# Performance work log

Hardware: AMD Instinct MI355X
Metric: run time of the kernel (lower is better)

Reference implementation:

```python
import jax, jax.numpy as jnp
import numpy as np

def mish(x):
    return x * jnp.tanh(jax.nn.softplus(x))

def setup_inputs() -> dict:
    ANT, RF, DS, G, B = 64, 8, 8, 16, 4096
    BB_DIM = 2 * RF * DS      # 128
    RF_DIM = 2 * ANT * RF     # 1024
    key = jax.random.key(0)
    ks = jax.random.split(key, 10)
    def lin(kw, kb, i, o):
        lim = 1.0 / np.sqrt(i)
        W = jax.random.uniform(kw, (o, i), jnp.float32, -lim, lim)
        b = jax.random.uniform(kb, (o,), jnp.float32, -lim, lim)
        return W, b
    W_rfbb, b_rfbb = lin(ks[0], ks[1], RF_DIM, BB_DIM)
    W_rfrf, b_rfrf = lin(ks[2], ks[3], RF_DIM, RF_DIM)
    W_bbrf, b_bbrf = lin(ks[4], ks[5], BB_DIM, RF_DIM)
    W_bbbb, b_bbbb = lin(ks[6], ks[7], BB_DIM, BB_DIM)
    BB_feature = jax.random.normal(ks[8], (B, G, BB_DIM), jnp.float32)
    RF_feature = jax.random.normal(ks[9], (B, RF_DIM), jnp.float32)
    return {
        "BB_feature": BB_feature, "RF_feature": RF_feature,
        "W_rfbb": W_rfbb, "b_rfbb": b_rfbb,
        "W_rfrf": W_rfrf, "b_rfrf": b_rfrf,
        "W_bbrf": W_bbrf, "b_bbrf": b_bbrf,
        "W_bbbb": W_bbbb, "b_bbbb": b_bbbb,
    }

def reference(BB_feature, RF_feature, W_rfbb, b_rfbb, W_rfrf, b_rfrf, W_bbrf, b_bbrf, W_bbbb, b_bbbb):
    # mean over subcarrier-group dim
    BB_mean = jnp.mean(BB_feature, axis=-2)                      # [B, BB_DIM]
    RF_to_RF = mish(RF_feature @ W_rfrf.T + b_rfrf)              # [B, RF_DIM]
    RF_to_BB = mish(RF_feature @ W_rfbb.T + b_rfbb)              # [B, BB_DIM]
    BB_to_RF = mish(BB_mean @ W_bbrf.T + b_bbrf)                 # [B, RF_DIM]
    BB_to_BB = mish(jnp.einsum('bgi,oi->bgo', BB_feature, W_bbbb) + b_bbbb)  # [B, G, BB_DIM]
    new_RF = RF_to_RF + BB_to_RF
    new_BB = BB_to_BB + RF_to_BB[:, None, :]
    return (new_BB, new_RF)
```

## Files before the change

kernel.cpp:

```cpp
#include <hip/hip_runtime.h>
#include <hip/hip_bf16.h>

typedef __attribute__((ext_vector_type(8))) short short8;
typedef __attribute__((ext_vector_type(4))) float floatx4;

#define BDIM 128
#define RDIM 1024
#define NB   4096
#define NG   16
#define LDP  40

__device__ __forceinline__ float mishf(float x) {
    float e = __expf(x);
    float t = e * (e + 2.0f);
    float r = x * (t / (t + 2.0f));
    return x > 20.0f ? x : r;
}

__device__ __forceinline__ short8 cvt8v(float4 f0, float4 f1) {
    union { __hip_bfloat162 h; unsigned u; } c0, c1, c2, c3;
    c0.h = __float22bfloat162_rn(make_float2(f0.x, f0.y));
    c1.h = __float22bfloat162_rn(make_float2(f0.z, f0.w));
    c2.h = __float22bfloat162_rn(make_float2(f1.x, f1.y));
    c3.h = __float22bfloat162_rn(make_float2(f1.z, f1.w));
    union { short8 s; unsigned u[4]; } r;
    r.u[0] = c0.u; r.u[1] = c1.u; r.u[2] = c2.u; r.u[3] = c3.u;
    return r.s;
}

#define MFMA(a, b, c) __builtin_amdgcn_mfma_f32_16x16x32_bf16(a, b, c, 0, 0, 0)

__global__ void __launch_bounds__(256) k_mean(const float* __restrict__ bb,
                                              float* __restrict__ mean) {
    int tid = blockIdx.x * blockDim.x + threadIdx.x;
    int b = tid >> 5;
    int d = (tid & 31) * 4;
    const float4* p = (const float4*)(bb + (size_t)b * (NG * BDIM) + d);
    float4 s = {0.f, 0.f, 0.f, 0.f};
    #pragma unroll
    for (int g = 0; g < NG; ++g) {
        float4 v = p[g * (BDIM / 4)];
        s.x += v.x; s.y += v.y; s.z += v.z; s.w += v.w;
    }
    s.x *= 0.0625f; s.y *= 0.0625f; s.z *= 0.0625f; s.w *= 0.0625f;
    *(float4*)(mean + (size_t)b * BDIM + d) = s;
}

__global__ void __launch_bounds__(256) k_rf2bb(
    const float* __restrict__ rf,
    const float* __restrict__ W,
    const float* __restrict__ bias,
    float* __restrict__ outw)
{
    __shared__ short As[16 * LDP];
    __shared__ short Bs[128 * LDP];
    int tid = threadIdx.x;
    int wave = tid >> 6, lane = tid & 63;
    int r = lane & 15, quad = lane >> 4;
    int m0 = blockIdx.x * 16;
    int srow = tid >> 2, sks = tid & 3;

    const float* aG  = rf + (size_t)(m0 + srow) * RDIM + sks * 8;
    const float* bG0 = W  + (size_t)srow * RDIM + sks * 8;
    const float* bG1 = W  + (size_t)(64 + srow) * RDIM + sks * 8;

    float4 qa0, qa1, qb00, qb01, qb10, qb11;
    if (tid < 64) { qa0 = *(const float4*)aG; qa1 = *(const float4*)(aG + 4); }
    qb00 = *(const float4*)bG0; qb01 = *(const float4*)(bG0 + 4);
    qb10 = *(const float4*)bG1; qb11 = *(const float4*)(bG1 + 4);

    floatx4 acc[2];
    acc[0] = floatx4{0.f,0.f,0.f,0.f}; acc[1] = acc[0];

    for (int it = 0; it < 32; ++it) {
        __syncthreads();
        if (tid < 64) *(short8*)&As[srow * LDP + sks * 8] = cvt8v(qa0, qa1);
        *(short8*)&Bs[srow * LDP + sks * 8]        = cvt8v(qb00, qb01);
        *(short8*)&Bs[(64 + srow) * LDP + sks * 8] = cvt8v(qb10, qb11);
        __syncthreads();
        if (it < 31) {
            int k = (it + 1) * 32;
            if (tid < 64) { qa0 = *(const float4*)(aG + k); qa1 = *(const float4*)(aG + k + 4); }
            qb00 = *(const float4*)(bG0 + k); qb01 = *(const float4*)(bG0 + k + 4);
            qb10 = *(const float4*)(bG1 + k); qb11 = *(const float4*)(bG1 + k + 4);
        }
        short8 a = *(short8*)&As[r * LDP + quad * 8];
        #pragma unroll
        for (int nj = 0; nj < 2; ++nj) {
            short8 b = *(short8*)&Bs[(wave * 32 + nj * 16 + r) * LDP + quad * 8];
            acc[nj] = MFMA(a, b, acc[nj]);
        }
    }
    #pragma unroll
    for (int nj = 0; nj < 2; ++nj) {
        int col = wave * 32 + nj * 16 + r;
        float bs = bias[col];
        #pragma unroll
        for (int g = 0; g < 4; ++g) {
            int row = m0 + quad * 4 + g;
            outw[(size_t)row * BDIM + col] = mishf(acc[nj][g] + bs);
        }
    }
}

__global__ void __launch_bounds__(512) k_newrf(
    const float* __restrict__ rf,
    const float* __restrict__ meanp,
    const float* __restrict__ Wrfrf,
    const float* __restrict__ brfrf,
    const float* __restrict__ Wbbrf,
    const float* __restrict__ bbbrf,
    float* __restrict__ out)
{
    __shared__ short As[128 * LDP];
    __shared__ short Bs[128 * LDP];
    int tid = threadIdx.x;
    int wave = tid >> 6, lane = tid & 63;
    int r = lane & 15, quad = lane >> 4;
    int w_m = (wave & 3) * 32, w_n = (wave >> 2) * 64;
    int mt = blockIdx.x >> 3, nt = blockIdx.x & 7;
    int m0 = mt * 128, n0 = nt * 128;
    int srow = tid >> 2, sks = tid & 3;
    int sidx = srow * LDP + sks * 8;

    const float* aG = rf    + (size_t)(m0 + srow) * RDIM + sks * 8;
    const float* bG = Wrfrf + (size_t)(n0 + srow) * RDIM + sks * 8;
    float4 pa0 = *(const float4*)aG, pa1 = *(const float4*)(aG + 4);
    float4 pb0 = *(const float4*)bG, pb1 = *(const float4*)(bG + 4);

    floatx4 acc1[2][4], acc2[2][4];
    #pragma unroll
    for (int i = 0; i < 2; ++i)
        #pragma unroll
        for (int j = 0; j < 4; ++j) { acc1[i][j] = floatx4{0.f,0.f,0.f,0.f}; acc2[i][j] = acc1[i][j]; }

    for (int it = 0; it < 32; ++it) {
        __syncthreads();
        *(short8*)&As[sidx] = cvt8v(pa0, pa1);
        *(short8*)&Bs[sidx] = cvt8v(pb0, pb1);
        __syncthreads();
        if (it < 31) {
            int k = (it + 1) * 32;
            pa0 = *(const float4*)(aG + k); pa1 = *(const float4*)(aG + k + 4);
            pb0 = *(const float4*)(bG + k); pb1 = *(const float4*)(bG + k + 4);
        }
        short8 a0 = *(short8*)&As[(w_m + r) * LDP + quad * 8];
        short8 a1 = *(short8*)&As[(w_m + 16 + r) * LDP + quad * 8];
        #pragma unroll
        for (int nj = 0; nj < 4; ++nj) {
            short8 b = *(short8*)&Bs[(w_n + nj * 16 + r) * LDP + quad * 8];
            acc1[0][nj] = MFMA(a0, b, acc1[0][nj]);
            acc1[1][nj] = MFMA(a1, b, acc1[1][nj]);
        }
    }

    const float* a2G = meanp + (size_t)(m0 + srow) * BDIM + sks * 8;
    const float* b2G = Wbbrf + (size_t)(n0 + srow) * BDIM + sks * 8;
    pa0 = *(const float4*)a2G; pa1 = *(const float4*)(a2G + 4);
    pb0 = *(const float4*)b2G; pb1 = *(const float4*)(b2G + 4);
    for (int it = 0; it < 4; ++it) {
        __syncthreads();
        *(short8*)&As[sidx] = cvt8v(pa0, pa1);
        *(short8*)&Bs[sidx] = cvt8v(pb0, pb1);
        __syncthreads();
        if (it < 3) {
            int k = (it + 1) * 32;
            pa0 = *(const float4*)(a2G + k); pa1 = *(const float4*)(a2G + k + 4);
            pb0 = *(const float4*)(b2G + k); pb1 = *(const float4*)(b2G + k + 4);
        }
        short8 a0 = *(short8*)&As[(w_m + r) * LDP + quad * 8];
        short8 a1 = *(short8*)&As[(w_m + 16 + r) * LDP + quad * 8];
        #pragma unroll
        for (int nj = 0; nj < 4; ++nj) {
            short8 b = *(short8*)&Bs[(w_n + nj * 16 + r) * LDP + quad * 8];
            acc2[0][nj] = MFMA(a0, b, acc2[0][nj]);
            acc2[1][nj] = MFMA(a1, b, acc2[1][nj]);
        }
    }

    #pragma unroll
    for (int mi = 0; mi < 2; ++mi) {
        #pragma unroll
        for (int nj = 0; nj < 4; ++nj) {
            int col = n0 + w_n + nj * 16 + r;
            float b1 = brfrf[col];
            float b2 = bbbrf[col];
            #pragma unroll
            for (int g = 0; g < 4; ++g) {
                int row = m0 + w_m + mi * 16 + quad * 4 + g;
                out[(size_t)row * RDIM + col] = mishf(acc1[mi][nj][g] + b1) + mishf(acc2[mi][nj][g] + b2);
            }
        }
    }
}

__global__ void __launch_bounds__(256) k_newbb(
    const float* __restrict__ bb,
    const float* __restrict__ W,
    const float* __restrict__ bias,
    const float* __restrict__ rf2bb,
    float* __restrict__ out)
{
    __shared__ short As[128 * LDP];
    __shared__ short Ws[128 * LDP];
    int tid = threadIdx.x;
    int wave = tid >> 6, lane = tid & 63;
    int r = lane & 15, quad = lane >> 4;
    size_t m0 = (size_t)blockIdx.x * 128;
    int srow = tid >> 2, sks = tid & 3;

    const float* aG0 = bb + (m0 + srow) * BDIM + sks * 8;
    const float* aG1 = bb + (m0 + 64 + srow) * BDIM + sks * 8;
    const float* wG0 = W + (size_t)srow * BDIM + sks * 8;
    const float* wG1 = W + (size_t)(64 + srow) * BDIM + sks * 8;

    float4 qa00 = *(const float4*)aG0, qa01 = *(const float4*)(aG0 + 4);
    float4 qa10 = *(const float4*)aG1, qa11 = *(const float4*)(aG1 + 4);
    float4 qw00 = *(const float4*)wG0, qw01 = *(const float4*)(wG0 + 4);
    float4 qw10 = *(const float4*)wG1, qw11 = *(const float4*)(wG1 + 4);

    floatx4 acc[2][8];
    #pragma unroll
    for (int i = 0; i < 2; ++i)
        #pragma unroll
        for (int j = 0; j < 8; ++j) acc[i][j] = floatx4{0.f,0.f,0.f,0.f};

    for (int kc = 0; kc < 4; ++kc) {
        __syncthreads();
        *(short8*)&As[srow * LDP + sks * 8]        = cvt8v(qa00, qa01);
        *(short8*)&As[(64 + srow) * LDP + sks * 8] = cvt8v(qa10, qa11);
        *(short8*)&Ws[srow * LDP + sks * 8]        = cvt8v(qw00, qw01);
        *(short8*)&Ws[(64 + srow) * LDP + sks * 8] = cvt8v(qw10, qw11);
        __syncthreads();
        if (kc < 3) {
            int k = (kc + 1) * 32;
            qa00 = *(const float4*)(aG0 + k); qa01 = *(const float4*)(aG0 + k + 4);
            qa10 = *(const float4*)(aG1 + k); qa11 = *(const float4*)(aG1 + k + 4);
            qw00 = *(const float4*)(wG0 + k); qw01 = *(const float4*)(wG0 + k + 4);
            qw10 = *(const float4*)(wG1 + k); qw11 = *(const float4*)(wG1 + k + 4);
        }
        short8 a0 = *(short8*)&As[(wave * 32 + r) * LDP + quad * 8];
        short8 a1 = *(short8*)&As[(wave * 32 + 16 + r) * LDP + quad * 8];
        #pragma unroll
        for (int nj = 0; nj < 8; ++nj) {
            short8 b = *(short8*)&Ws[(nj * 16 + r) * LDP + quad * 8];
            acc[0][nj] = MFMA(a0, b, acc[0][nj]);
            acc[1][nj] = MFMA(a1, b, acc[1][nj]);
        }
    }

    #pragma unroll
    for (int mi = 0; mi < 2; ++mi) {
        #pragma unroll
        for (int nj = 0; nj < 8; ++nj) {
            int col = nj * 16 + r;
            float bs = bias[col];
            #pragma unroll
            for (int g = 0; g < 4; ++g) {
                size_t row = m0 + wave * 32 + mi * 16 + quad * 4 + g;
                out[row * BDIM + col] = mishf(acc[mi][nj][g] + bs) + rf2bb[(row >> 4) * BDIM + col];
            }
        }
    }
}

extern "C" void kernel_launch(void* const* d_in, const int* in_sizes, int n_in,
                              void* d_out, int out_size, void* d_ws, size_t ws_size,
                              hipStream_t stream) {
    const float* BB    = (const float*)d_in[0];
    const float* RF    = (const float*)d_in[1];
    const float* Wrfbb = (const float*)d_in[2];
    const float* brfbb = (const float*)d_in[3];
    const float* Wrfrf = (const float*)d_in[4];
    const float* brfrf = (const float*)d_in[5];
    const float* Wbbrf = (const float*)d_in[6];
    const float* bbbrf = (const float*)d_in[7];
    const float* Wbbbb = (const float*)d_in[8];
    const float* bbbbb = (const float*)d_in[9];

    float* outBB = (float*)d_out;
    float* outRF = outBB + (size_t)NB * NG * BDIM;

    float* mean  = (float*)d_ws;
    float* rf2bb = (float*)((char*)d_ws + (size_t)NB * BDIM * 4);

    k_mean <<<512, 256, 0, stream>>>(BB, mean);
    k_rf2bb<<<256, 256, 0, stream>>>(RF, Wrfbb, brfbb, rf2bb);
    k_newrf<<<256, 512, 0, stream>>>(RF, mean, Wrfrf, brfrf, Wbbrf, bbbrf, outRF);
    k_newbb<<<512, 256, 0, stream>>>(BB, Wbbbb, bbbbb, rf2bb, outBB);
}
```

Before: 187.8 us.

## Fuse RF-to-BB GEMM into RF GEMM kernel and double-buffer LDS tiles

Removes the separate k_rf2bb kernel: the first 8 column tiles of k_newrf also compute the RF→BB projection, reusing the already-staged RF A-tiles against a 16-row slice of W_rfbb. The RF kernel's tiling changes to 128x64 tiles with 256 threads and 512 blocks, and LDS becomes double-buffered so each k-step needs one barrier instead of two. k_newbb now stages the full W_bbbb once into LDS and double-buffers only the activation tiles. The cost is load imbalance, since only half of the RF blocks and half of their waves do the extra MFMA work, plus more LDS per block.

Measured after the change: 162.6 us. 1.15x faster.

```diff
diff --git a/kernel.cpp b/kernel.cpp
--- a/kernel.cpp
+++ b/kernel.cpp
@@ -9,6 +9,7 @@
 #define NB   4096
 #define NG   16
 #define LDP  40
+#define WSTR 136
 
 __device__ __forceinline__ float mishf(float x) {
     float e = __expf(x);
@@ -46,149 +47,167 @@
     *(float4*)(mean + (size_t)b * BDIM + d) = s;
 }
 
-__global__ void __launch_bounds__(256) k_rf2bb(
-    const float* __restrict__ rf,
-    const float* __restrict__ W,
-    const float* __restrict__ bias,
-    float* __restrict__ outw)
-{
-    __shared__ short As[16 * LDP];
-    __shared__ short Bs[128 * LDP];
-    int tid = threadIdx.x;
-    int wave = tid >> 6, lane = tid & 63;
-    int r = lane & 15, quad = lane >> 4;
-    int m0 = blockIdx.x * 16;
-    int srow = tid >> 2, sks = tid & 3;
-
-    const float* aG  = rf + (size_t)(m0 + srow) * RDIM + sks * 8;
-    const float* bG0 = W  + (size_t)srow * RDIM + sks * 8;
-    const float* bG1 = W  + (size_t)(64 + srow) * RDIM + sks * 8;
-
-    float4 qa0, qa1, qb00, qb01, qb10, qb11;
-    if (tid < 64) { qa0 = *(const float4*)aG; qa1 = *(const float4*)(aG + 4); }
-    qb00 = *(const float4*)bG0; qb01 = *(const float4*)(bG0 + 4);
-    qb10 = *(const float4*)bG1; qb11 = *(const float4*)(bG1 + 4);
-
-    floatx4 acc[2];
-    acc[0] = floatx4{0.f,0.f,0.f,0.f}; acc[1] = acc[0];
-
-    for (int it = 0; it < 32; ++it) {
-        __syncthreads();
-        if (tid < 64) *(short8*)&As[srow * LDP + sks * 8] = cvt8v(qa0, qa1);
-        *(short8*)&Bs[srow * LDP + sks * 8]        = cvt8v(qb00, qb01);
-        *(short8*)&Bs[(64 + srow) * LDP + sks * 8] = cvt8v(qb10, qb11);
-        __syncthreads();
-        if (it < 31) {
-            int k = (it + 1) * 32;
-            if (tid < 64) { qa0 = *(const float4*)(aG + k); qa1 = *(const float4*)(aG + k + 4); }
-            qb00 = *(const float4*)(bG0 + k); qb01 = *(const float4*)(bG0 + k + 4);
-            qb10 = *(const float4*)(bG1 + k); qb11 = *(const float4*)(bG1 + k + 4);
-        }
-        short8 a = *(short8*)&As[r * LDP + quad * 8];
-        #pragma unroll
-        for (int nj = 0; nj < 2; ++nj) {
-            short8 b = *(short8*)&Bs[(wave * 32 + nj * 16 + r) * LDP + quad * 8];
-            acc[nj] = MFMA(a, b, acc[nj]);
-        }
-    }
-    #pragma unroll
-    for (int nj = 0; nj < 2; ++nj) {
-        int col = wave * 32 + nj * 16 + r;
-        float bs = bias[col];
-        #pragma unroll
-        for (int g = 0; g < 4; ++g) {
-            int row = m0 + quad * 4 + g;
-            outw[(size_t)row * BDIM + col] = mishf(acc[nj][g] + bs);
-        }
-    }
-}
-
-__global__ void __launch_bounds__(512) k_newrf(
+__global__ void __launch_bounds__(256) k_newrf(
     const float* __restrict__ rf,
     const float* __restrict__ meanp,
     const float* __restrict__ Wrfrf,
     const float* __restrict__ brfrf,
     const float* __restrict__ Wbbrf,
     const float* __restrict__ bbbrf,
-    float* __restrict__ out)
+    const float* __restrict__ Wrfbb,
+    const float* __restrict__ brfbb,
+    float* __restrict__ out,
+    float* __restrict__ rf2bb)
 {
-    __shared__ short As[128 * LDP];
-    __shared__ short Bs[128 * LDP];
+    __shared__ short As[2][128 * LDP];
+    __shared__ short Bs[2][64 * LDP];
+    __shared__ short Ws2[2][16 * LDP];
     int tid = threadIdx.x;
     int wave = tid >> 6, lane = tid & 63;
     int r = lane & 15, quad = lane >> 4;
-    int w_m = (wave & 3) * 32, w_n = (wave >> 2) * 64;
-    int mt = blockIdx.x >> 3, nt = blockIdx.x & 7;
-    int m0 = mt * 128, n0 = nt * 128;
-    int srow = tid >> 2, sks = tid & 3;
-    int sidx = srow * LDP + sks * 8;
-
-    const float* aG = rf    + (size_t)(m0 + srow) * RDIM + sks * 8;
-    const float* bG = Wrfrf + (size_t)(n0 + srow) * RDIM + sks * 8;
-    float4 pa0 = *(const float4*)aG, pa1 = *(const float4*)(aG + 4);
-    float4 pb0 = *(const float4*)bG, pb1 = *(const float4*)(bG + 4);
-
-    floatx4 acc1[2][4], acc2[2][4];
-    #pragma unroll
-    for (int i = 0; i < 2; ++i)
-        #pragma unroll
-        for (int j = 0; j < 4; ++j) { acc1[i][j] = floatx4{0.f,0.f,0.f,0.f}; acc2[i][j] = acc1[i][j]; }
+    int wm = (wave & 1) * 64, wn = (wave >> 1) * 32;
+    int mt = blockIdx.x >> 4, nt = blockIdx.x & 15;
+    int m0 = mt * 128, n0 = nt * 64;
+    bool doP = (nt < 8);
+
+    int arow = tid >> 1, akh = (tid & 1) * 16;
+    int brow = tid >> 2, bkq = (tid & 3) * 8;
+    int aidx = arow * LDP + akh;
+    int bidx = brow * LDP + bkq;
+    int widx = (tid >> 2) * LDP + bkq;
+
+    const float* aG = rf    + (size_t)(m0 + arow) * RDIM + akh;
+    const float* bG = Wrfrf + (size_t)(n0 + brow) * RDIM + bkq;
+    const float* wG = Wrfbb + (size_t)(nt * 16 + (tid >> 2)) * RDIM + bkq;
+
+    floatx4 acc1[4][2], acc2[4][2], acc3[4];
+    #pragma unroll
+    for (int mi = 0; mi < 4; ++mi) {
+        acc1[mi][0] = floatx4{0.f,0.f,0.f,0.f}; acc1[mi][1] = acc1[mi][0];
+        acc2[mi][0] = acc1[mi][0]; acc2[mi][1] = acc1[mi][0];
+        acc3[mi] = acc1[mi][0];
+    }
+    float4 ra0, ra1, ra2, ra3, rb0, rb1, rw0, rw1;
+    bool wload = doP && (tid < 64);
+
+    ra0 = ((const float4*)aG)[0]; ra1 = ((const float4*)aG)[1];
+    ra2 = ((const float4*)aG)[2]; ra3 = ((const float4*)aG)[3];
+    rb0 = ((const float4*)bG)[0]; rb1 = ((const float4*)bG)[1];
+    if (wload) { rw0 = ((const float4*)wG)[0]; rw1 = ((const float4*)wG)[1]; }
+    *(short8*)&As[0][aidx]     = cvt8v(ra0, ra1);
+    *(short8*)&As[0][aidx + 8] = cvt8v(ra2, ra3);
+    *(short8*)&Bs[0][bidx]     = cvt8v(rb0, rb1);
+    if (wload) *(short8*)&Ws2[0][widx] = cvt8v(rw0, rw1);
+    ra0 = ((const float4*)(aG + 32))[0]; ra1 = ((const float4*)(aG + 32))[1];
+    ra2 = ((const float4*)(aG + 32))[2]; ra3 = ((const float4*)(aG + 32))[3];
+    rb0 = ((const float4*)(bG + 32))[0]; rb1 = ((const float4*)(bG + 32))[1];
+    if (wload) { rw0 = ((const float4*)(wG + 32))[0]; rw1 = ((const float4*)(wG + 32))[1]; }
+    __syncthreads();
 
     for (int it = 0; it < 32; ++it) {
+        const short* Ac = As[it & 1];
+        const short* Bc = Bs[it & 1];
+        const short* Wc = Ws2[it & 1];
+        short8 af[4];
+        #pragma unroll
+        for (int mi = 0; mi < 4; ++mi)
+            af[mi] = *(const short8*)&Ac[(wm + mi * 16 + r) * LDP + quad * 8];
+        short8 bf[2];
+        bf[0] = *(const short8*)&Bc[(wn + r) * LDP + quad * 8];
+        bf[1] = *(const short8*)&Bc[(wn + 16 + r) * LDP + quad * 8];
+        #pragma unroll
+        for (int mi = 0; mi < 4; ++mi) {
+            acc1[mi][0] = MFMA(af[mi], bf[0], acc1[mi][0]);
+            acc1[mi][1] = MFMA(af[mi], bf[1], acc1[mi][1]);
+        }
+        if (doP && (wave & 2) == 0) {
+            short8 b2 = *(const short8*)&Wc[r * LDP + quad * 8];
+            #pragma unroll
+            for (int mi = 0; mi < 4; ++mi) acc3[mi] = MFMA(af[mi], b2, acc3[mi]);
+        }
+        if (it < 31) {
+            int nb = (it + 1) & 1;
+            *(short8*)&As[nb][aidx]     = cvt8v(ra0, ra1);
+            *(short8*)&As[nb][aidx + 8] = cvt8v(ra2, ra3);
+            *(short8*)&Bs[nb][bidx]     = cvt8v(rb0, rb1);
+            if (wload) *(short8*)&Ws2[nb][widx] = cvt8v(rw0, rw1);
+        }
+        if (it < 30) {
+            int k = (it + 2) * 32;
+            ra0 = ((const float4*)(aG + k))[0]; ra1 = ((const float4*)(aG + k))[1];
+            ra2 = ((const float4*)(aG + k))[2]; ra3 = ((const float4*)(aG + k))[3];
+            rb0 = ((const float4*)(bG + k))[0]; rb1 = ((const float4*)(bG + k))[1];
+            if (wload) { rw0 = ((const float4*)(wG + k))[0]; rw1 = ((const float4*)(wG + k))[1]; }
+        }
         __syncthreads();
-        *(short8*)&As[sidx] = cvt8v(pa0, pa1);
-        *(short8*)&Bs[sidx] = cvt8v(pb0, pb1);
+    }
+
+    const float* a2G = meanp + (size_t)(m0 + arow) * BDIM + akh;
+    const float* b2G = Wbbrf + (size_t)(n0 + brow) * BDIM + bkq;
+    ra0 = ((const float4*)a2G)[0]; ra1 = ((const float4*)a2G)[1];
+    ra2 = ((const float4*)a2G)[2]; ra3 = ((const float4*)a2G)[3];
+    rb0 = ((const float4*)b2G)[0]; rb1 = ((const float4*)b2G)[1];
+    *(short8*)&As[0][aidx]     = cvt8v(ra0, ra1);
+    *(short8*)&As[0][aidx + 8] = cvt8v(ra2, ra3);
+    *(short8*)&Bs[0][bidx]     = cvt8v(rb0, rb1);
+    ra0 = ((const float4*)(a2G + 32))[0]; ra1 = ((const float4*)(a2G + 32))[1];
+    ra2 = ((const float4*)(a2G + 32))[2]; ra3 = ((const float4*)(a2G + 32))[3];
+    rb0 = ((const float4*)(b2G + 32))[0]; rb1 = ((const float4*)(b2G + 32))[1];
+    __syncthreads();
+    for (int it = 0; it < 4; ++it) {
+        const short* Ac = As[it & 1];
+        const short* Bc = Bs[it & 1];
+        short8 af[4];
+        #pragma unroll
+        for (int mi = 0; mi < 4; ++mi)
+            af[mi] = *(const short8*)&Ac[(wm + mi * 16 + r) * LDP + quad * 8];
+        short8 bf[2];
+        bf[0] = *(const short8*)&Bc[(wn + r) * LDP + quad * 8];
+        bf[1] = *(const short8*)&Bc[(wn + 16 + r) * LDP + quad * 8];
+        #pragma unroll
+        for (int mi = 0; mi < 4; ++mi) {
+            acc2[mi][0] = MFMA(af[mi], bf[0], acc2[mi][0]);
+            acc2[mi][1] = MFMA(af[mi], bf[1], acc2[mi][1]);
+        }
+        if (it < 3) {
+            int nb = (it + 1) & 1;
+            *(short8*)&As[nb][aidx]     = cvt8v(ra0, ra1);
+            *(short8*)&As[nb][aidx + 8] = cvt8v(ra2, ra3);
+            *(short8*)&Bs[nb][bidx]     = cvt8v(rb0, rb1);
+        }
+        if (it < 2) {
+            int k = (it + 2) * 32;
+            ra0 = ((const float4*)(a2G + k))[0]; ra1 = ((const float4*)(a2G + k))[1];
+            ra2 = ((const float4*)(a2G + k))[2]; ra3 = ((const float4*)(a2G + k))[3];
+            rb0 = ((const float4*)(b2G + k))[0]; rb1 = ((const float4*)(b2G + k))[1];
+        }
         __syncthreads();
-        if (it < 31) {
-            int k = (it + 1) * 32;
-            pa0 = *(const float4*)(aG + k); pa1 = *(const float4*)(aG + k + 4);
-            pb0 = *(const float4*)(bG + k); pb1 = *(const float4*)(bG + k + 4);
-        }
-        short8 a0 = *(short8*)&As[(w_m + r) * LDP + quad * 8];
-        short8 a1 = *(short8*)&As[(w_m + 16 + r) * LDP + quad * 8];
-        #pragma unroll
-        for (int nj = 0; nj < 4; ++nj) {
-            short8 b = *(short8*)&Bs[(w_n + nj * 16 + r) * LDP + quad * 8];
-            acc1[0][nj] = MFMA(a0, b, acc1[0][nj]);
-            acc1[1][nj] = MFMA(a1, b, acc1[1][nj]);
-        }
-    }
-
-    const float* a2G = meanp + (size_t)(m0 + srow) * BDIM + sks * 8;
-    const float* b2G = Wbbrf + (size_t)(n0 + srow) * BDIM + sks * 8;
-    pa0 = *(const float4*)a2G; pa1 = *(const float4*)(a2G + 4);
-    pb0 = *(const float4*)b2G; pb1 = *(const float4*)(b2G + 4);
-    for (int it = 0; it < 4; ++it) {
-        __syncthreads();
-        *(short8*)&As[sidx] = cvt8v(pa0, pa1);
-        *(short8*)&Bs[sidx] = cvt8v(pb0, pb1);
-        __syncthreads();
-        if (it < 3) {
-            int k = (it + 1) * 32;
-            pa0 = *(const float4*)(a2G + k); pa1 = *(const float4*)(a2G + k + 4);
-            pb0 = *(const float4*)(b2G + k); pb1 = *(const float4*)(b2G + k + 4);
-        }
-        short8 a0 = *(short8*)&As[(w_m + r) * LDP + quad * 8];
-        short8 a1 = *(short8*)&As[(w_m + 16 + r) * LDP + quad * 8];
-        #pragma unroll
-        for (int nj = 0; nj < 4; ++nj) {
-            short8 b = *(short8*)&Bs[(w_n + nj * 16 + r) * LDP + quad * 8];
-            acc2[0][nj] = MFMA(a0, b, acc2[0][nj]);
-            acc2[1][nj] = MFMA(a1, b, acc2[1][nj]);
-        }
-    }
-
-    #pragma unroll
-    for (int mi = 0; mi < 2; ++mi) {
-        #pragma unroll
-        for (int nj = 0; nj < 4; ++nj) {
-            int col = n0 + w_n + nj * 16 + r;
-            float b1 = brfrf[col];
-            float b2 = bbbrf[col];
+    }
+
+    #pragma unroll
+    for (int nj = 0; nj < 2; ++nj) {
+        int col = n0 + wn + nj * 16 + r;
+        float b1 = brfrf[col];
+        float b2 = bbbrf[col];
+        #pragma unroll
+        for (int mi = 0; mi < 4; ++mi) {
             #pragma unroll
             for (int g = 0; g < 4; ++g) {
-                int row = m0 + w_m + mi * 16 + quad * 4 + g;
-                out[(size_t)row * RDIM + col] = mishf(acc1[mi][nj][g] + b1) + mishf(acc2[mi][nj][g] + b2);
+                int row = m0 + wm + mi * 16 + quad * 4 + g;
+                out[(size_t)row * RDIM + col] =
+                    mishf(acc1[mi][nj][g] + b1) + mishf(acc2[mi][nj][g] + b2);
+            }
+        }
+    }
+    if (doP && (wave & 2) == 0) {
+        int col = nt * 16 + r;
+        float bs = brfbb[col];
+        #pragma unroll
+        for (int mi = 0; mi < 4; ++mi) {
+            #pragma unroll
+            for (int g = 0; g < 4; ++g) {
+                int row = m0 + wm + mi * 16 + quad * 4 + g;
+                rf2bb[(size_t)row * BDIM + col] = mishf(acc3[mi][g] + bs);
             }
         }
     }
@@ -201,23 +220,27 @@
     const float* __restrict__ rf2bb,
     float* __restrict__ out)
 {
-    __shared__ short As[128 * LDP];
-    __shared__ short Ws[128 * LDP];
+    __shared__ short Wt[128 * WSTR];
+    __shared__ short As[2][128 * LDP];
     int tid = threadIdx.x;
     int wave = tid >> 6, lane = tid & 63;
     int r = lane & 15, quad = lane >> 4;
     size_t m0 = (size_t)blockIdx.x * 128;
-    int srow = tid >> 2, sks = tid & 3;
-
-    const float* aG0 = bb + (m0 + srow) * BDIM + sks * 8;
-    const float* aG1 = bb + (m0 + 64 + srow) * BDIM + sks * 8;
-    const float* wG0 = W + (size_t)srow * BDIM + sks * 8;
-    const float* wG1 = W + (size_t)(64 + srow) * BDIM + sks * 8;
-
-    float4 qa00 = *(const float4*)aG0, qa01 = *(const float4*)(aG0 + 4);
-    float4 qa10 = *(const float4*)aG1, qa11 = *(const float4*)(aG1 + 4);
-    float4 qw00 = *(const float4*)wG0, qw01 = *(const float4*)(wG0 + 4);
-    float4 qw10 = *(const float4*)wG1, qw11 = *(const float4*)(wG1 + 4);
+
+    {
+        int row = tid >> 1, half = (tid & 1) * 64;
+        const float* wp = W + (size_t)row * BDIM + half;
+        #pragma unroll
+        for (int j = 0; j < 8; ++j) {
+            float4 f0 = ((const float4*)(wp + j * 8))[0];
+            float4 f1 = ((const float4*)(wp + j * 8))[1];
+            *(short8*)&Wt[row * WSTR + half + j * 8] = cvt8v(f0, f1);
+        }
+    }
+
+    int arow = tid >> 1, akh = (tid & 1) * 16;
+    int aidx = arow * LDP + akh;
+    const float* aG = bb + (m0 + arow) * BDIM + akh;
 
     floatx4 acc[2][8];
     #pragma unroll
@@ -225,28 +248,36 @@
         #pragma unroll
         for (int j = 0; j < 8; ++j) acc[i][j] = floatx4{0.f,0.f,0.f,0.f};
 
+    float4 ra0, ra1, ra2, ra3;
+    ra0 = ((const float4*)aG)[0]; ra1 = ((const float4*)aG)[1];
+    ra2 = ((const float4*)aG)[2]; ra3 = ((const float4*)aG)[3];
+    *(short8*)&As[0][aidx]     = cvt8v(ra0, ra1);
+    *(short8*)&As[0][aidx + 8] = cvt8v(ra2, ra3);
+    ra0 = ((const float4*)(aG + 32))[0]; ra1 = ((const float4*)(aG + 32))[1];
+    ra2 = ((const float4*)(aG + 32))[2]; ra3 = ((const float4*)(aG + 32))[3];
+    __syncthreads();
+
     for (int kc = 0; kc < 4; ++kc) {
-        __syncthreads();
-        *(short8*)&As[srow * LDP + sks * 8]        = cvt8v(qa00, qa01);
-        *(short8*)&As[(64 + srow) * LDP + sks * 8] = cvt8v(qa10, qa11);
-        *(short8*)&Ws[srow * LDP + sks * 8]        = cvt8v(qw00, qw01);
-        *(short8*)&Ws[(64 + srow) * LDP + sks * 8] = cvt8v(qw10, qw11);
-        __syncthreads();
-        if (kc < 3) {
-            int k = (kc + 1) * 32;
-            qa00 = *(const float4*)(aG0 + k); qa01 = *(const float4*)(aG0 + k + 4);
-            qa10 = *(const float4*)(aG1 + k); qa11 = *(const float4*)(aG1 + k + 4);
-            qw00 = *(const float4*)(wG0 + k); qw01 = *(const float4*)(wG0 + k + 4);
-            qw10 = *(const float4*)(wG1 + k); qw11 = *(const float4*)(wG1 + k + 4);
-        }
-        short8 a0 = *(short8*)&As[(wave * 32 + r) * LDP + quad * 8];
-        short8 a1 = *(short8*)&As[(wave * 32 + 16 + r) * LDP + quad * 8];
+        const short* Ac = As[kc & 1];
+        short8 a0 = *(const short8*)&Ac[(wave * 32 + r) * LDP + quad * 8];
+        short8 a1 = *(const short8*)&Ac[(wave * 32 + 16 + r) * LDP + quad * 8];
         #pragma unroll
         for (int nj = 0; nj < 8; ++nj) {
-            short8 b = *(short8*)&Ws[(nj * 16 + r) * LDP + quad * 8];
+            short8 b = *(const short8*)&Wt[(nj * 16 + r) * WSTR + kc * 32 + quad * 8];
             acc[0][nj] = MFMA(a0, b, acc[0][nj]);
             acc[1][nj] = MFMA(a1, b, acc[1][nj]);
         }
+        if (kc < 3) {
+            int nb = (kc + 1) & 1;
+            *(short8*)&As[nb][aidx]     = cvt8v(ra0, ra1);
+            *(short8*)&As[nb][aidx + 8] = cvt8v(ra2, ra3);
+        }
+        if (kc < 2) {
+            int k = (kc + 2) * 32;
+            ra0 = ((const float4*)(aG + k))[0]; ra1 = ((const float4*)(aG + k))[1];
+            ra2 = ((const float4*)(aG + k))[2]; ra3 = ((const float4*)(aG + k))[3];
+        }
+        __syncthreads();
     }
 
     #pragma unroll
@@ -285,7 +316,7 @@
     float* rf2bb = (float*)((char*)d_ws + (size_t)NB * BDIM * 4);
 
     k_mean <<<512, 256, 0, stream>>>(BB, mean);
-    k_rf2bb<<<256, 256, 0, stream>>>(RF, Wrfbb, brfbb, rf2bb);
-    k_newrf<<<256, 512, 0, stream>>>(RF, mean, Wrfrf, brfrf, Wbbrf, bbbrf, outRF);
+    k_newrf<<<512, 256, 0, stream>>>(RF, mean, Wrfrf, brfrf, Wbbrf, bbbrf,
+                                     Wrfbb, brfbb, outRF, rf2bb);
     k_newbb<<<512, 256, 0, stream>>>(BB, Wbbbb, bbbbb, rf2bb, outBB);
 }
```
